# Kernel tuning notes

Hardware: AMD Instinct MI355X
Metric: run time of the kernel (lower is better)

The kernel has to match this reference:

```python
import jax, jax.numpy as jnp
import numpy as np

N_HEAD = 9
HEAD_DIM = 64
KV_PER_HEAD = 21  # 189 // 9
ROPE_BASE = 10000.0


def _rotate_half(x):
    # matches torch: x1 = first half (floor), x2 = rest; cat(-x2, x1)
    h = x.shape[-1] // 2
    return jnp.concatenate([-x[..., h:], x[..., :h]], axis=-1)


def _rope_cos_sin(T, dtype):
    inv_freq = 1.0 / (ROPE_BASE ** (jnp.arange(0, KV_PER_HEAD, 2, dtype=jnp.float32) / KV_PER_HEAD))  # [11]
    t = jnp.arange(T, dtype=jnp.float32)
    freqs = jnp.einsum('i,j->ij', t, inv_freq)          # [T, 11]
    emb = jnp.concatenate([freqs, freqs], axis=-1)      # [T, 22]
    cos = jnp.cos(emb)[:, :KV_PER_HEAD].astype(dtype)   # [T, 21]
    sin = jnp.sin(emb)[:, :KV_PER_HEAD].astype(dtype)
    return cos, sin


def setup_inputs() -> dict:
    key = jax.random.key(0)
    ks = jax.random.split(key, 5)
    B, T, C = 4, 2048, 576
    kv_dim = 189
    s = 0.02
    return {
        'x': jax.random.normal(ks[0], (B, T, C), dtype=jnp.float32),
        'Wq': jax.random.normal(ks[1], (C, C), dtype=jnp.float32) * s,
        'Wk': jax.random.normal(ks[2], (C, kv_dim), dtype=jnp.float32) * s,
        'Wv': jax.random.normal(ks[3], (C, kv_dim), dtype=jnp.float32) * s,
        'Wo': jax.random.normal(ks[4], (C, C), dtype=jnp.float32) * s,
    }


def reference(x, Wq, Wk, Wv, Wo):
    B, T, C = x.shape
    q = (x @ Wq).reshape(B, T, N_HEAD, HEAD_DIM).transpose(0, 2, 1, 3)      # [B,H,T,64]
    k = (x @ Wk).reshape(B, T, N_HEAD, KV_PER_HEAD).transpose(0, 2, 1, 3)   # [B,H,T,21]
    v = (x @ Wv).reshape(B, T, N_HEAD, KV_PER_HEAD).transpose(0, 2, 1, 3)   # [B,H,T,21]

    cos, sin = _rope_cos_sin(T, x.dtype)  # [T,21] each, broadcasts over B,H
    k_rot = k * cos + _rotate_half(k) * sin
    q_part = q[..., :KV_PER_HEAD]
    q_rot_part = q_part * cos + _rotate_half(q_part) * sin
    # q dims >= KV_PER_HEAD never touch nonzero K, so only the first 21 dims matter
    scale = 1.0 / np.sqrt(HEAD_DIM)
    scores = jnp.einsum('bhqd,bhkd->bhqk', q_rot_part, k_rot) * scale       # [B,H,T,T]
    causal = jnp.tril(jnp.ones((T, T), dtype=bool))
    scores = jnp.where(causal, scores, -1e9)
    attn = jax.nn.softmax(scores, axis=-1)
    y_small = jnp.einsum('bhqk,bhkd->bhqd', attn, v)                        # [B,H,T,21]
    # zero-pad up to head_dim (matches k_pad/v_pad construction)
    y = jnp.pad(y_small, ((0, 0), (0, 0), (0, 0), (0, HEAD_DIM - KV_PER_HEAD)))
    y = y.transpose(0, 2, 1, 3).reshape(B, T, C)
    return y @ Wo
```

## Files before the change

### kernel.cpp

```cpp
#include <hip/hip_runtime.h>
#include <hip/hip_bf16.h>

typedef unsigned short u16;
typedef unsigned int u32;
typedef __attribute__((ext_vector_type(8))) short bf16x8;
typedef __attribute__((ext_vector_type(4))) float f32x4;
typedef __attribute__((ext_vector_type(4))) int i32x4;

#define N_HEADS 9
#define T_SEQ 2048
#define BATCH 4
#define CDIM 576
#define ROWS (BATCH * T_SEQ)
#define NBH (BATCH * N_HEADS)
#define PART_SLOT ((size_t)NBH * T_SEQ * 32)

__device__ __forceinline__ u16 f2bf(float f) {
    u32 u = __float_as_uint(f);
    u32 r = u + 0x7FFFu + ((u >> 16) & 1u);
    return (u16)(r >> 16);
}
__device__ __forceinline__ float bf2f(u16 u) { return __uint_as_float(((u32)u) << 16); }
__device__ __forceinline__ u32 cvt_pk_bf16(float lo, float hi) {
    u32 r;
    asm("v_cvt_pk_bf16_f32 %0, %1, %2" : "=v"(r) : "v"(lo), "v"(hi));
    return r;
}
__device__ __forceinline__ float exp2_raw(float x) {
    float r;
    asm("v_exp_f32 %0, %1" : "=v"(r) : "v"(x));
    return r;
}

__global__ __launch_bounds__(256) void prep_wt(const float* __restrict__ Wq, const float* __restrict__ Wk,
                                               const float* __restrict__ Wv, const float* __restrict__ Wo,
                                               u16* __restrict__ WcT, u16* __restrict__ WoSubT,
                                               float* __restrict__ cosT, float* __restrict__ sinT) {
    int idx = blockIdx.x * 256 + threadIdx.x;
    if (idx < 576 * 576) {
        int n = idx / 576, k = idx - n * 576;
        float v;
        if (n < 189)      v = Wq[(size_t)k * 576 + (n / 21) * 64 + (n % 21)];
        else if (n < 378) v = Wk[(size_t)k * 189 + (n - 189)];
        else if (n < 567) v = Wv[(size_t)k * 189 + (n - 378)];
        else              v = 0.f;
        WcT[(size_t)n * 576 + k] = f2bf(v);
    }
    if (idx < 576 * 192) {
        int n = idx / 192, k = idx - n * 192;
        float v = 0.f;
        if (k < 189) v = Wo[(size_t)((k / 21) * 64 + (k % 21)) * 576 + n];
        WoSubT[(size_t)n * 192 + k] = f2bf(v);
    }
    if (idx < T_SEQ * 21) {
        int t = idx / 21, d = idx - t * 21;
        int i = (d < 11) ? d : d - 11;
        float e = (2.0f * (float)i) / 21.0f;
        float invf = exp2f(-e * 13.287712379549449f);
        float ang = (float)t * invf;
        cosT[idx] = cosf(ang);
        sinT[idx] = sinf(ang);
    }
}


template <int AF32, int OUTF32>
__global__ __launch_bounds__(256) void gemm_mfma(const void* __restrict__ Av, const u16* __restrict__ BT,
                                                 void* __restrict__ Cout, int K, int lda, int ldbt, int ldc) {
    __shared__ u16 As[128][32];
    __shared__ u16 Bs[64][32];
    const int tid = threadIdx.x;
    const int lane = tid & 63, w = tid >> 6;
    const int m0 = (blockIdx.x & 63) * 128, n0 = (blockIdx.x >> 6) * 64;
    const int k15 = lane & 15, g = lane >> 4;

    const int arow = tid >> 1;
    const int ac0 = (tid & 1) * 2;
    const int brow = tid >> 2, bc = tid & 3;

    f32x4 zero = {0.f, 0.f, 0.f, 0.f};
    f32x4 acc[2][4];
#pragma unroll
    for (int hf = 0; hf < 2; hf++)
#pragma unroll
        for (int n = 0; n < 4; n++) acc[hf][n] = zero;

    const float* Af = (const float*)Av;
    const u16*   Ab = (const u16*)Av;

    float4 af0, af1, af2, af3;
    i32x4 av0, av1;
    if (AF32) {
        const float* ap = &Af[(size_t)(m0 + arow) * lda + ac0 * 8];
        af0 = *(const float4*)&ap[0];
        af1 = *(const float4*)&ap[4];
        af2 = *(const float4*)&ap[8];
        af3 = *(const float4*)&ap[12];
    } else {
        av0 = *(const i32x4*)&Ab[(size_t)(m0 + arow) * lda + ac0 * 8];
        av1 = *(const i32x4*)&Ab[(size_t)(m0 + arow) * lda + (ac0 + 1) * 8];
    }
    i32x4 bv = *(const i32x4*)&BT[(size_t)(n0 + brow) * ldbt + bc * 8];

    for (int k0 = 0; k0 < K; k0 += 32) {
        __syncthreads();
        if (AF32) {
            i32x4 w0, w1;
            w0[0] = (int)cvt_pk_bf16(af0.x, af0.y); w0[1] = (int)cvt_pk_bf16(af0.z, af0.w);
            w0[2] = (int)cvt_pk_bf16(af1.x, af1.y); w0[3] = (int)cvt_pk_bf16(af1.z, af1.w);
            w1[0] = (int)cvt_pk_bf16(af2.x, af2.y); w1[1] = (int)cvt_pk_bf16(af2.z, af2.w);
            w1[2] = (int)cvt_pk_bf16(af3.x, af3.y); w1[3] = (int)cvt_pk_bf16(af3.z, af3.w);
            *(i32x4*)&As[arow][(ac0 ^ (arow & 3)) * 8] = w0;
            *(i32x4*)&As[arow][((ac0 + 1) ^ (arow & 3)) * 8] = w1;
        } else {
            *(i32x4*)&As[arow][(ac0 ^ (arow & 3)) * 8] = av0;
            *(i32x4*)&As[arow][((ac0 + 1) ^ (arow & 3)) * 8] = av1;
        }
        *(i32x4*)&Bs[brow][(bc ^ (brow & 3)) * 8] = bv;
        __syncthreads();
        int k1 = k0 + 32;
        if (k1 < K) {
            if (AF32) {
                const float* ap = &Af[(size_t)(m0 + arow) * lda + k1 + ac0 * 8];
                af0 = *(const float4*)&ap[0];
                af1 = *(const float4*)&ap[4];
                af2 = *(const float4*)&ap[8];
                af3 = *(const float4*)&ap[12];
            } else {
                av0 = *(const i32x4*)&Ab[(size_t)(m0 + arow) * lda + k1 + ac0 * 8];
                av1 = *(const i32x4*)&Ab[(size_t)(m0 + arow) * lda + k1 + (ac0 + 1) * 8];
            }
            bv = *(const i32x4*)&BT[(size_t)(n0 + brow) * ldbt + k1 + bc * 8];
        }
        const int ar0 = w * 32 + k15;
        bf16x8 a0 = *(const bf16x8*)&As[ar0][(g ^ (ar0 & 3)) * 8];
        bf16x8 a1 = *(const bf16x8*)&As[ar0 + 16][(g ^ (ar0 & 3)) * 8];
#pragma unroll
        for (int n = 0; n < 4; n++) {
            int br = n * 16 + k15;
            bf16x8 b = *(const bf16x8*)&Bs[br][(g ^ (br & 3)) * 8];
            acc[0][n] = __builtin_amdgcn_mfma_f32_16x16x32_bf16(a0, b, acc[0][n], 0, 0, 0);
            acc[1][n] = __builtin_amdgcn_mfma_f32_16x16x32_bf16(a1, b, acc[1][n], 0, 0, 0);
        }
    }
#pragma unroll
    for (int hf = 0; hf < 2; hf++)
#pragma unroll
        for (int n = 0; n < 4; n++)
#pragma unroll
            for (int i = 0; i < 4; i++) {
                int row = m0 + w * 32 + hf * 16 + g * 4 + i;
                int col = n0 + n * 16 + k15;
                float v = acc[hf][n][i];
                if (OUTF32) ((float*)Cout)[(size_t)row * ldc + col] = v;
                else        ((u16*)Cout)[(size_t)row * ldc + col] = f2bf(v);
            }
}


__global__ __launch_bounds__(256) void repack_qkv(const u16* __restrict__ qkv,
                                                  const float* __restrict__ cosT,
                                                  const float* __restrict__ sinT,
                                                  u16* __restrict__ Qp, u16* __restrict__ Kp,
                                                  u16* __restrict__ Vp) {
    __shared__ u16 Qs[64][40];
    __shared__ u16 Ksh[64][40];
    __shared__ u16 Vsh[64][40];
    const int tid = threadIdx.x;
    const int bh = blockIdx.y;
    const int b = bh / N_HEADS, h = bh - b * N_HEADS;
    const int t0 = blockIdx.x * 64;

    const int qa = (h * 21) & ~7,        qoff = h * 21 - qa;
    const int ka = (189 + h * 21) & ~7,  koff = 189 + h * 21 - ka;
    const int va = (378 + h * 21) & ~7,  voff = 378 + h * 21 - va;

#pragma unroll
    for (int it = 0; it < 3; ++it) {
        int idx = tid + it * 256;
        int row = idx / 12;
        int r12 = idx - row * 12;
        int stream = r12 >> 2, chunk = r12 & 3;
        int off = (stream == 0) ? qa : (stream == 1) ? ka : va;
        const u16* src = qkv + (size_t)(b * T_SEQ + t0 + row) * CDIM + off + chunk * 8;
        i32x4 v = *(const i32x4*)src;
        u16* dst = (stream == 0) ? &Qs[row][0] : (stream == 1) ? &Ksh[row][0] : &Vsh[row][0];
        *(i32x4*)&dst[chunk * 8] = v;
    }
    __syncthreads();

    const int r = tid >> 2, c = tid & 3;
    const int t = t0 + r;
    const float* cr = cosT + t * 21;
    const float* sr = sinT + t * 21;
    u32 wq[4] = {0, 0, 0, 0}, wk[4] = {0, 0, 0, 0};
    const float sc = 0.18033688011112042f;
#pragma unroll
    for (int j = 0; j < 8; j++) {
        int d = c * 8 + j;
        float vq = 0.f, vk = 0.f;
        if (d < 21) {
            int pd = (d < 11) ? d + 10 : d - 11;
            float cc = cr[d], ss = sr[d];
            float qv = bf2f(Qs[r][qoff + d]),  qp = bf2f(Qs[r][qoff + pd]);
            float kv = bf2f(Ksh[r][koff + d]), kp = bf2f(Ksh[r][koff + pd]);
            float rq = (d < 11) ? -qp : qp;
            float rk = (d < 11) ? -kp : kp;
            vq = (qv * cc + rq * ss) * sc;
            vk = kv * cc + rk * ss;
        }
        wq[j >> 1] |= (u32)f2bf(vq) << ((j & 1) * 16);
        wk[j >> 1] |= (u32)f2bf(vk) << ((j & 1) * 16);
    }
    size_t obase = ((size_t)bh * T_SEQ + t) * 32 + c * 8;
    i32x4 q4; q4[0] = (int)wq[0]; q4[1] = (int)wq[1]; q4[2] = (int)wq[2]; q4[3] = (int)wq[3];
    i32x4 k4; k4[0] = (int)wk[0]; k4[1] = (int)wk[1]; k4[2] = (int)wk[2]; k4[3] = (int)wk[3];
    *(i32x4*)&Qp[obase] = q4;
    *(i32x4*)&Kp[obase] = k4;

    const int dv = tid >> 3, tc = tid & 7;
    u32 wv[4];
#pragma unroll
    for (int j = 0; j < 4; j++) {
        u16 lo, hi;
        if (dv < 21)      { lo = Vsh[tc * 8 + j * 2][voff + dv]; hi = Vsh[tc * 8 + j * 2 + 1][voff + dv]; }
        else if (dv == 31){ lo = 0x3F80; hi = 0x3F80; }
        else              { lo = 0; hi = 0; }
        wv[j] = (u32)lo | ((u32)hi << 16);
    }
    i32x4 v4; v4[0] = (int)wv[0]; v4[1] = (int)wv[1]; v4[2] = (int)wv[2]; v4[3] = (int)wv[3];
    *(i32x4*)&Vp[((size_t)bh * 32 + dv) * T_SEQ + t0 + tc * 8] = v4;
}


__global__ __launch_bounds__(512) void attn_mfma(const u16* __restrict__ Qp,
                                                 const u16* __restrict__ Kp,
                                                 const u16* __restrict__ Vp,
                                                 u16* __restrict__ Ybuf,
                                                 u16* __restrict__ Part) {
    __shared__ u16 Ks[2][128][40];
    __shared__ u16 Vt[2][32][136];
    __shared__ u16 Pt[2][8][16][72];
    const int tid = threadIdx.x;
    const int lane = tid & 63, w = tid >> 6;
    const int bh = blockIdx.y;
    const int b = bh / N_HEADS, h = bh - b * N_HEADS;
    const int k15 = lane & 15, g = lane >> 4;

    int qt2 = 15, ci = blockIdx.x;
    for (int q = 15; q >= 0; --q) {
        int n = (q >> 2) + 1;
        if (ci < n) { qt2 = q; break; }
        ci -= n;
    }
    const int q0 = qt2 * 128;
    const int n128 = qt2 + 1;
    const int nc = (qt2 >> 2) + 1;
    const int u_begin = (ci * n128) / nc;
    const int u_end = ((ci + 1) * n128) / nc;

    const bool isK = (tid < 256);
    const int krow = (tid & 255) >> 2, kc = tid & 3;
    const int vrow = (tid & 255) >> 3, vc = tid & 7;
    const u16* Kg = Kp + (size_t)bh * 65536 + krow * 32 + kc * 8;
    const u16* Vg = Vp + (size_t)bh * 65536 + vrow * 2048 + vc * 8;

    bf16x8 qf = *(const bf16x8*)&Qp[(((size_t)bh << 11) + q0 + w * 16 + k15) * 32 + g * 8];

    f32x4 y0 = {0.f, 0.f, 0.f, 0.f}, y1 = {0.f, 0.f, 0.f, 0.f};
    const int qloc = (w & 3) * 16 + k15;
    const int kd = 2 * qt2 + (w >> 2);

    u32 koff = (u32)u_begin * 4096u;
    u32 voffu = (u32)u_begin * 128u;
    i32x4 r0, r1;
    if (isK) { r0 = *(const i32x4*)&Kg[koff];   r1 = *(const i32x4*)&Kg[koff + 2048]; }
    else     { r0 = *(const i32x4*)&Vg[voffu];  r1 = *(const i32x4*)&Vg[voffu + 64]; }
    if (isK) {
        *(i32x4*)&Ks[0][krow][kc * 8] = r0;
        *(i32x4*)&Ks[0][krow + 64][kc * 8] = r1;
    } else {
        *(i32x4*)&Vt[0][vrow][vc * 8] = r0;
        *(i32x4*)&Vt[0][vrow][vc * 8 + 64] = r1;
    }
    if (u_begin + 1 < u_end) {
        koff += 4096u; voffu += 128u;
        if (isK) { r0 = *(const i32x4*)&Kg[koff];   r1 = *(const i32x4*)&Kg[koff + 2048]; }
        else     { r0 = *(const i32x4*)&Vg[voffu];  r1 = *(const i32x4*)&Vg[voffu + 64]; }
    }

    int cur = 0;
    for (int u = u_begin; u < u_end; ++u) {
        __syncthreads();
        if (u + 1 < u_end) {
            if (isK) {
                *(i32x4*)&Ks[cur ^ 1][krow][kc * 8] = r0;
                *(i32x4*)&Ks[cur ^ 1][krow + 64][kc * 8] = r1;
            } else {
                *(i32x4*)&Vt[cur ^ 1][vrow][vc * 8] = r0;
                *(i32x4*)&Vt[cur ^ 1][vrow][vc * 8 + 64] = r1;
            }
            if (u + 2 < u_end) {
                koff += 4096u; voffu += 128u;
                if (isK) { r0 = *(const i32x4*)&Kg[koff];   r1 = *(const i32x4*)&Kg[koff + 2048]; }
                else     { r0 = *(const i32x4*)&Vg[voffu];  r1 = *(const i32x4*)&Vg[voffu + 64]; }
            }
        }

        const int kt0 = u * 2;
        const bool do0 = (kt0 <= kd);
        const bool do1 = (kt0 + 1 <= kd);

        if (do0) {
            f32x4 s0[4], s1[4];
            __builtin_amdgcn_s_setprio(1);
#pragma unroll
            for (int f = 0; f < 4; f++) {
                bf16x8 kf = *(const bf16x8*)&Ks[cur][f * 16 + k15][g * 8];
                f32x4 z = {0.f, 0.f, 0.f, 0.f};
                s0[f] = __builtin_amdgcn_mfma_f32_16x16x32_bf16(kf, qf, z, 0, 0, 0);
            }
            if (do1) {
#pragma unroll
                for (int f = 0; f < 4; f++) {
                    bf16x8 kf = *(const bf16x8*)&Ks[cur][64 + f * 16 + k15][g * 8];
                    f32x4 z = {0.f, 0.f, 0.f, 0.f};
                    s1[f] = __builtin_amdgcn_mfma_f32_16x16x32_bf16(kf, qf, z, 0, 0, 0);
                }
            }
            __builtin_amdgcn_s_setprio(0);

            if (kt0 == kd) {
#pragma unroll
                for (int f = 0; f < 4; f++)
#pragma unroll
                    for (int i = 0; i < 4; i++)
                        if (f * 16 + g * 4 + i > qloc) s0[f][i] = -16384.f;
            }
            if (do1 && kt0 + 1 == kd) {
#pragma unroll
                for (int f = 0; f < 4; f++)
#pragma unroll
                    for (int i = 0; i < 4; i++)
                        if (f * 16 + g * 4 + i > qloc) s1[f][i] = -16384.f;
            }

#pragma unroll
            for (int f = 0; f < 4; f++) {
                u32 lo = cvt_pk_bf16(exp2_raw(s0[f][0]), exp2_raw(s0[f][1]));
                u32 hi = cvt_pk_bf16(exp2_raw(s0[f][2]), exp2_raw(s0[f][3]));
                uint2 pk; pk.x = lo; pk.y = hi;
                *(uint2*)&Pt[0][w][k15][f * 16 + g * 4] = pk;
            }
            if (do1) {
#pragma unroll
                for (int f = 0; f < 4; f++) {
                    u32 lo = cvt_pk_bf16(exp2_raw(s1[f][0]), exp2_raw(s1[f][1]));
                    u32 hi = cvt_pk_bf16(exp2_raw(s1[f][2]), exp2_raw(s1[f][3]));
                    uint2 pk; pk.x = lo; pk.y = hi;
                    *(uint2*)&Pt[1][w][k15][f * 16 + g * 4] = pk;
                }
            }
            asm volatile("" ::: "memory");

            __builtin_amdgcn_s_setprio(1);
#pragma unroll
            for (int kh = 0; kh < 2; kh++) {
                bf16x8 pa = *(const bf16x8*)&Pt[0][w][k15][kh * 32 + g * 8];
                bf16x8 v0 = *(const bf16x8*)&Vt[cur][k15][kh * 32 + g * 8];
                bf16x8 v1 = *(const bf16x8*)&Vt[cur][16 + k15][kh * 32 + g * 8];
                y0 = __builtin_amdgcn_mfma_f32_16x16x32_bf16(pa, v0, y0, 0, 0, 0);
                y1 = __builtin_amdgcn_mfma_f32_16x16x32_bf16(pa, v1, y1, 0, 0, 0);
            }
            if (do1) {
#pragma unroll
                for (int kh = 0; kh < 2; kh++) {
                    bf16x8 pa = *(const bf16x8*)&Pt[1][w][k15][kh * 32 + g * 8];
                    bf16x8 v0 = *(const bf16x8*)&Vt[cur][k15][64 + kh * 32 + g * 8];
                    bf16x8 v1 = *(const bf16x8*)&Vt[cur][16 + k15][64 + kh * 32 + g * 8];
                    y0 = __builtin_amdgcn_mfma_f32_16x16x32_bf16(pa, v0, y0, 0, 0, 0);
                    y1 = __builtin_amdgcn_mfma_f32_16x16x32_bf16(pa, v1, y1, 0, 0, 0);
                }
            }
            __builtin_amdgcn_s_setprio(0);
            asm volatile("" ::: "memory");
        }
        cur ^= 1;
    }

    if (nc == 1) {
#pragma unroll
        for (int i = 0; i < 4; i++) {
            float li = __shfl(y1[i], (lane & 48) + 15);
            float inv = 1.0f / li;
            int rowY = b * T_SEQ + q0 + w * 16 + g * 4 + i;
            u16* yr = &Ybuf[(size_t)rowY * 192 + h * 21];
            yr[k15] = f2bf(y0[i] * inv);
            if (k15 < 5) yr[16 + k15] = f2bf(y1[i] * inv);
        }
    } else {
#pragma unroll
        for (int i = 0; i < 4; i++) {
            size_t pb = (size_t)ci * PART_SLOT +
                        (((size_t)bh << 11) + q0 + w * 16 + g * 4 + i) * 32;
            Part[pb + k15] = f2bf(y0[i]);
            Part[pb + 16 + k15] = f2bf(y1[i]);
        }
    }
}

__global__ __launch_bounds__(256) void attn_reduce(const u16* __restrict__ Part, u16* __restrict__ Ybuf) {
    int gid = blockIdx.x * 256 + threadIdx.x;
    int d = gid & 31;
    int rest = gid >> 5;
    int t = 512 + (rest % 1536);
    int bh = rest / 1536;
    int b = bh / N_HEADS, h = bh - b * N_HEADS;
    int nc = (t >> 9) + 1;
    size_t base = (((size_t)bh << 11) + t) * 32;
    float l = 0.f, v = 0.f;
    for (int ci = 0; ci < nc; ci++) {
        l += bf2f(Part[(size_t)ci * PART_SLOT + base + 31]);
        if (d < 21) v += bf2f(Part[(size_t)ci * PART_SLOT + base + d]);
    }
    if (d < 21) Ybuf[(size_t)(b * T_SEQ + t) * 192 + h * 21 + d] = f2bf(v / l);
}


extern "C" void kernel_launch(void* const* d_in, const int* in_sizes, int n_in,
                              void* d_out, int out_size, void* d_ws, size_t ws_size,
                              hipStream_t stream) {
    const float* x  = (const float*)d_in[0];
    const float* Wq = (const float*)d_in[1];
    const float* Wk = (const float*)d_in[2];
    const float* Wv = (const float*)d_in[3];
    const float* Wo = (const float*)d_in[4];
    float* out = (float*)d_out;

    char* p = (char*)d_ws;
    auto alloc = [&](size_t bytes) { char* r = p; p += (bytes + 255) & ~(size_t)255; return r; };
    u16*   QpKp   = (u16*)alloc((size_t)ROWS * CDIM * 2);
    u16*   qkv    = (u16*)alloc((size_t)ROWS * CDIM * 2);
    u16*   WcT    = (u16*)alloc((size_t)576 * 576 * 2);
    u16*   WoSubT = (u16*)alloc((size_t)576 * 192 * 2);
    float* cosT   = (float*)alloc((size_t)T_SEQ * 21 * 4);
    float* sinT   = (float*)alloc((size_t)T_SEQ * 21 * 4);
    u16*   Vp     = (u16*)alloc((size_t)NBH * 32 * T_SEQ * 2);
    u16*   Ybuf   = (u16*)alloc((size_t)ROWS * 192 * 2);
    u16*   Part   = (u16*)alloc((size_t)4 * PART_SLOT * 2);

    u16* Qp = QpKp;
    u16* Kp = QpKp + (size_t)NBH * T_SEQ * 32;

    prep_wt<<<dim3((576 * 576 + 255) / 256), dim3(256), 0, stream>>>(Wq, Wk, Wv, Wo, WcT, WoSubT, cosT, sinT);

    gemm_mfma<1, 0><<<dim3(64 * 9), dim3(256), 0, stream>>>((const void*)x, WcT, (void*)qkv, 576, 576, 576, 576);

    repack_qkv<<<dim3(T_SEQ / 64, NBH), dim3(256), 0, stream>>>(qkv, cosT, sinT, Qp, Kp, Vp);

    attn_mfma<<<dim3(40, NBH), dim3(512), 0, stream>>>(Qp, Kp, Vp, Ybuf, Part);
    attn_reduce<<<dim3(NBH * 1536 * 32 / 256), dim3(256), 0, stream>>>(Part, Ybuf);

    gemm_mfma<0, 1><<<dim3(64 * 9), dim3(256), 0, stream>>>((const void*)Ybuf, WoSubT, (void*)out, 192, 192, 192, 576);
}
```

Before: 77.88 us.

## Halve attention block to 4 waves, each handling two 16-row query fragments

The attention kernel now launches 256 threads instead of 512, and each wave processes 32 query rows as two 16-row fragments. Every K fragment loaded from shared memory and every V fragment is reused across both query fragments. Each thread now loads both K and V for the tile, where before threads were split between the two. This cuts LDS reads per MFMA and keeps more MFMAs in flight per wave, at the cost of more registers per thread and fewer waves per block available to hide latency.

Measured after the change: 79.58 us. 2.2% more time.

```diff
diff --git a/kernel.cpp b/kernel.cpp
--- a/kernel.cpp
+++ b/kernel.cpp
@@ -233,14 +233,14 @@
 }
 
 
-__global__ __launch_bounds__(512) void attn_mfma(const u16* __restrict__ Qp,
+__global__ __launch_bounds__(256) void attn_mfma(const u16* __restrict__ Qp,
                                                  const u16* __restrict__ Kp,
                                                  const u16* __restrict__ Vp,
                                                  u16* __restrict__ Ybuf,
                                                  u16* __restrict__ Part) {
     __shared__ u16 Ks[2][128][40];
     __shared__ u16 Vt[2][32][136];
-    __shared__ u16 Pt[2][8][16][72];
+    __shared__ u16 Pt[2][4][2][16][72];
     const int tid = threadIdx.x;
     const int lane = tid & 63, w = tid >> 6;
     const int bh = blockIdx.y;
@@ -259,152 +259,139 @@
     const int u_begin = (ci * n128) / nc;
     const int u_end = ((ci + 1) * n128) / nc;
 
-    const bool isK = (tid < 256);
-    const int krow = (tid & 255) >> 2, kc = tid & 3;
-    const int vrow = (tid & 255) >> 3, vc = tid & 7;
-    const u16* Kg = Kp + (size_t)bh * 65536 + krow * 32 + kc * 8;
+    const int krow = tid >> 1, kc = tid & 1;
+    const int vrow = tid >> 3, vc = tid & 7;
+    const u16* Kg = Kp + (size_t)bh * 65536 + krow * 32 + kc * 16;
     const u16* Vg = Vp + (size_t)bh * 65536 + vrow * 2048 + vc * 8;
 
-    bf16x8 qf = *(const bf16x8*)&Qp[(((size_t)bh << 11) + q0 + w * 16 + k15) * 32 + g * 8];
-
-    f32x4 y0 = {0.f, 0.f, 0.f, 0.f}, y1 = {0.f, 0.f, 0.f, 0.f};
-    const int qloc = (w & 3) * 16 + k15;
-    const int kd = 2 * qt2 + (w >> 2);
+    bf16x8 qfA = *(const bf16x8*)&Qp[(((size_t)bh << 11) + q0 + w * 32 + k15) * 32 + g * 8];
+    bf16x8 qfB = *(const bf16x8*)&Qp[(((size_t)bh << 11) + q0 + w * 32 + 16 + k15) * 32 + g * 8];
+
+    f32x4 y0A = {0.f, 0.f, 0.f, 0.f}, y1A = {0.f, 0.f, 0.f, 0.f};
+    f32x4 y0B = {0.f, 0.f, 0.f, 0.f}, y1B = {0.f, 0.f, 0.f, 0.f};
+    const int qlocA = ((2 * w) & 3) * 16 + k15;
+    const int qlocB = qlocA + 16;
+    const int kd = 2 * qt2 + (w >> 1);
 
     u32 koff = (u32)u_begin * 4096u;
     u32 voffu = (u32)u_begin * 128u;
-    i32x4 r0, r1;
-    if (isK) { r0 = *(const i32x4*)&Kg[koff];   r1 = *(const i32x4*)&Kg[koff + 2048]; }
-    else     { r0 = *(const i32x4*)&Vg[voffu];  r1 = *(const i32x4*)&Vg[voffu + 64]; }
-    if (isK) {
-        *(i32x4*)&Ks[0][krow][kc * 8] = r0;
-        *(i32x4*)&Ks[0][krow + 64][kc * 8] = r1;
-    } else {
-        *(i32x4*)&Vt[0][vrow][vc * 8] = r0;
-        *(i32x4*)&Vt[0][vrow][vc * 8 + 64] = r1;
-    }
+    i32x4 kr0 = *(const i32x4*)&Kg[koff];
+    i32x4 kr1 = *(const i32x4*)&Kg[koff + 8];
+    i32x4 vr0 = *(const i32x4*)&Vg[voffu];
+    i32x4 vr1 = *(const i32x4*)&Vg[voffu + 64];
+    *(i32x4*)&Ks[0][krow][kc * 16] = kr0;
+    *(i32x4*)&Ks[0][krow][kc * 16 + 8] = kr1;
+    *(i32x4*)&Vt[0][vrow][vc * 8] = vr0;
+    *(i32x4*)&Vt[0][vrow][vc * 8 + 64] = vr1;
     if (u_begin + 1 < u_end) {
         koff += 4096u; voffu += 128u;
-        if (isK) { r0 = *(const i32x4*)&Kg[koff];   r1 = *(const i32x4*)&Kg[koff + 2048]; }
-        else     { r0 = *(const i32x4*)&Vg[voffu];  r1 = *(const i32x4*)&Vg[voffu + 64]; }
+        kr0 = *(const i32x4*)&Kg[koff];
+        kr1 = *(const i32x4*)&Kg[koff + 8];
+        vr0 = *(const i32x4*)&Vg[voffu];
+        vr1 = *(const i32x4*)&Vg[voffu + 64];
     }
 
     int cur = 0;
     for (int u = u_begin; u < u_end; ++u) {
         __syncthreads();
         if (u + 1 < u_end) {
-            if (isK) {
-                *(i32x4*)&Ks[cur ^ 1][krow][kc * 8] = r0;
-                *(i32x4*)&Ks[cur ^ 1][krow + 64][kc * 8] = r1;
-            } else {
-                *(i32x4*)&Vt[cur ^ 1][vrow][vc * 8] = r0;
-                *(i32x4*)&Vt[cur ^ 1][vrow][vc * 8 + 64] = r1;
-            }
+            *(i32x4*)&Ks[cur ^ 1][krow][kc * 16] = kr0;
+            *(i32x4*)&Ks[cur ^ 1][krow][kc * 16 + 8] = kr1;
+            *(i32x4*)&Vt[cur ^ 1][vrow][vc * 8] = vr0;
+            *(i32x4*)&Vt[cur ^ 1][vrow][vc * 8 + 64] = vr1;
             if (u + 2 < u_end) {
                 koff += 4096u; voffu += 128u;
-                if (isK) { r0 = *(const i32x4*)&Kg[koff];   r1 = *(const i32x4*)&Kg[koff + 2048]; }
-                else     { r0 = *(const i32x4*)&Vg[voffu];  r1 = *(const i32x4*)&Vg[voffu + 64]; }
-            }
-        }
-
-        const int kt0 = u * 2;
-        const bool do0 = (kt0 <= kd);
-        const bool do1 = (kt0 + 1 <= kd);
-
-        if (do0) {
-            f32x4 s0[4], s1[4];
-            __builtin_amdgcn_s_setprio(1);
-#pragma unroll
-            for (int f = 0; f < 4; f++) {
-                bf16x8 kf = *(const bf16x8*)&Ks[cur][f * 16 + k15][g * 8];
-                f32x4 z = {0.f, 0.f, 0.f, 0.f};
-                s0[f] = __builtin_amdgcn_mfma_f32_16x16x32_bf16(kf, qf, z, 0, 0, 0);
-            }
-            if (do1) {
+                kr0 = *(const i32x4*)&Kg[koff];
+                kr1 = *(const i32x4*)&Kg[koff + 8];
+                vr0 = *(const i32x4*)&Vg[voffu];
+                vr1 = *(const i32x4*)&Vg[voffu + 64];
+            }
+        }
+
+#pragma unroll
+        for (int sub = 0; sub < 2; ++sub) {
+            const int kt = u * 2 + sub;
+            if (kt <= kd) {
+                f32x4 sA[4], sB[4];
+                __builtin_amdgcn_s_setprio(1);
 #pragma unroll
                 for (int f = 0; f < 4; f++) {
-                    bf16x8 kf = *(const bf16x8*)&Ks[cur][64 + f * 16 + k15][g * 8];
+                    bf16x8 kf = *(const bf16x8*)&Ks[cur][sub * 64 + f * 16 + k15][g * 8];
                     f32x4 z = {0.f, 0.f, 0.f, 0.f};
-                    s1[f] = __builtin_amdgcn_mfma_f32_16x16x32_bf16(kf, qf, z, 0, 0, 0);
+                    sA[f] = __builtin_amdgcn_mfma_f32_16x16x32_bf16(kf, qfA, z, 0, 0, 0);
+                    sB[f] = __builtin_amdgcn_mfma_f32_16x16x32_bf16(kf, qfB, z, 0, 0, 0);
                 }
-            }
-            __builtin_amdgcn_s_setprio(0);
-
-            if (kt0 == kd) {
-#pragma unroll
-                for (int f = 0; f < 4; f++)
-#pragma unroll
-                    for (int i = 0; i < 4; i++)
-                        if (f * 16 + g * 4 + i > qloc) s0[f][i] = -16384.f;
-            }
-            if (do1 && kt0 + 1 == kd) {
-#pragma unroll
-                for (int f = 0; f < 4; f++)
-#pragma unroll
-                    for (int i = 0; i < 4; i++)
-                        if (f * 16 + g * 4 + i > qloc) s1[f][i] = -16384.f;
-            }
-
-#pragma unroll
-            for (int f = 0; f < 4; f++) {
-                u32 lo = cvt_pk_bf16(exp2_raw(s0[f][0]), exp2_raw(s0[f][1]));
-                u32 hi = cvt_pk_bf16(exp2_raw(s0[f][2]), exp2_raw(s0[f][3]));
-                uint2 pk; pk.x = lo; pk.y = hi;
-                *(uint2*)&Pt[0][w][k15][f * 16 + g * 4] = pk;
-            }
-            if (do1) {
+                __builtin_amdgcn_s_setprio(0);
+
+                if (kt == kd) {
+#pragma unroll
+                    for (int f = 0; f < 4; f++)
+#pragma unroll
+                        for (int i = 0; i < 4; i++) {
+                            if (f * 16 + g * 4 + i > qlocA) sA[f][i] = -16384.f;
+                            if (f * 16 + g * 4 + i > qlocB) sB[f][i] = -16384.f;
+                        }
+                }
+
 #pragma unroll
                 for (int f = 0; f < 4; f++) {
-                    u32 lo = cvt_pk_bf16(exp2_raw(s1[f][0]), exp2_raw(s1[f][1]));
-                    u32 hi = cvt_pk_bf16(exp2_raw(s1[f][2]), exp2_raw(s1[f][3]));
-                    uint2 pk; pk.x = lo; pk.y = hi;
-                    *(uint2*)&Pt[1][w][k15][f * 16 + g * 4] = pk;
+                    u32 loA = cvt_pk_bf16(exp2_raw(sA[f][0]), exp2_raw(sA[f][1]));
+                    u32 hiA = cvt_pk_bf16(exp2_raw(sA[f][2]), exp2_raw(sA[f][3]));
+                    uint2 pkA; pkA.x = loA; pkA.y = hiA;
+                    *(uint2*)&Pt[sub][w][0][k15][f * 16 + g * 4] = pkA;
+                    u32 loB = cvt_pk_bf16(exp2_raw(sB[f][0]), exp2_raw(sB[f][1]));
+                    u32 hiB = cvt_pk_bf16(exp2_raw(sB[f][2]), exp2_raw(sB[f][3]));
+                    uint2 pkB; pkB.x = loB; pkB.y = hiB;
+                    *(uint2*)&Pt[sub][w][1][k15][f * 16 + g * 4] = pkB;
                 }
-            }
-            asm volatile("" ::: "memory");
-
-            __builtin_amdgcn_s_setprio(1);
-#pragma unroll
-            for (int kh = 0; kh < 2; kh++) {
-                bf16x8 pa = *(const bf16x8*)&Pt[0][w][k15][kh * 32 + g * 8];
-                bf16x8 v0 = *(const bf16x8*)&Vt[cur][k15][kh * 32 + g * 8];
-                bf16x8 v1 = *(const bf16x8*)&Vt[cur][16 + k15][kh * 32 + g * 8];
-                y0 = __builtin_amdgcn_mfma_f32_16x16x32_bf16(pa, v0, y0, 0, 0, 0);
-                y1 = __builtin_amdgcn_mfma_f32_16x16x32_bf16(pa, v1, y1, 0, 0, 0);
-            }
-            if (do1) {
+                asm volatile("" ::: "memory");
+
+                __builtin_amdgcn_s_setprio(1);
 #pragma unroll
                 for (int kh = 0; kh < 2; kh++) {
-                    bf16x8 pa = *(const bf16x8*)&Pt[1][w][k15][kh * 32 + g * 8];
-                    bf16x8 v0 = *(const bf16x8*)&Vt[cur][k15][64 + kh * 32 + g * 8];
-                    bf16x8 v1 = *(const bf16x8*)&Vt[cur][16 + k15][64 + kh * 32 + g * 8];
-                    y0 = __builtin_amdgcn_mfma_f32_16x16x32_bf16(pa, v0, y0, 0, 0, 0);
-                    y1 = __builtin_amdgcn_mfma_f32_16x16x32_bf16(pa, v1, y1, 0, 0, 0);
+                    bf16x8 paA = *(const bf16x8*)&Pt[sub][w][0][k15][kh * 32 + g * 8];
+                    bf16x8 paB = *(const bf16x8*)&Pt[sub][w][1][k15][kh * 32 + g * 8];
+                    bf16x8 v0 = *(const bf16x8*)&Vt[cur][k15][sub * 64 + kh * 32 + g * 8];
+                    bf16x8 v1 = *(const bf16x8*)&Vt[cur][16 + k15][sub * 64 + kh * 32 + g * 8];
+                    y0A = __builtin_amdgcn_mfma_f32_16x16x32_bf16(paA, v0, y0A, 0, 0, 0);
+                    y1A = __builtin_amdgcn_mfma_f32_16x16x32_bf16(paA, v1, y1A, 0, 0, 0);
+                    y0B = __builtin_amdgcn_mfma_f32_16x16x32_bf16(paB, v0, y0B, 0, 0, 0);
+                    y1B = __builtin_amdgcn_mfma_f32_16x16x32_bf16(paB, v1, y1B, 0, 0, 0);
                 }
-            }
-            __builtin_amdgcn_s_setprio(0);
-            asm volatile("" ::: "memory");
+                __builtin_amdgcn_s_setprio(0);
+                asm volatile("" ::: "memory");
+            }
         }
         cur ^= 1;
     }
 
     if (nc == 1) {
 #pragma unroll
-        for (int i = 0; i < 4; i++) {
-            float li = __shfl(y1[i], (lane & 48) + 15);
-            float inv = 1.0f / li;
-            int rowY = b * T_SEQ + q0 + w * 16 + g * 4 + i;
-            u16* yr = &Ybuf[(size_t)rowY * 192 + h * 21];
-            yr[k15] = f2bf(y0[i] * inv);
-            if (k15 < 5) yr[16 + k15] = f2bf(y1[i] * inv);
+        for (int fr = 0; fr < 2; fr++) {
+            f32x4 yy0 = fr ? y0B : y0A;
+            f32x4 yy1 = fr ? y1B : y1A;
+#pragma unroll
+            for (int i = 0; i < 4; i++) {
+                float li = __shfl(yy1[i], (lane & 48) + 15);
+                float inv = 1.0f / li;
+                int rowY = b * T_SEQ + q0 + w * 32 + fr * 16 + g * 4 + i;
+                u16* yr = &Ybuf[(size_t)rowY * 192 + h * 21];
+                yr[k15] = f2bf(yy0[i] * inv);
+                if (k15 < 5) yr[16 + k15] = f2bf(yy1[i] * inv);
+            }
         }
     } else {
 #pragma unroll
-        for (int i = 0; i < 4; i++) {
-            size_t pb = (size_t)ci * PART_SLOT +
-                        (((size_t)bh << 11) + q0 + w * 16 + g * 4 + i) * 32;
-            Part[pb + k15] = f2bf(y0[i]);
-            Part[pb + 16 + k15] = f2bf(y1[i]);
+        for (int fr = 0; fr < 2; fr++) {
+            f32x4 yy0 = fr ? y0B : y0A;
+            f32x4 yy1 = fr ? y1B : y1A;
+#pragma unroll
+            for (int i = 0; i < 4; i++) {
+                size_t pb = (size_t)ci * PART_SLOT +
+                            (((size_t)bh << 11) + q0 + w * 32 + fr * 16 + g * 4 + i) * 32;
+                Part[pb + k15] = f2bf(yy0[i]);
+                Part[pb + 16 + k15] = f2bf(yy1[i]);
+            }
         }
     }
 }
@@ -458,7 +445,7 @@
 
     repack_qkv<<<dim3(T_SEQ / 64, NBH), dim3(256), 0, stream>>>(qkv, cosT, sinT, Qp, Kp, Vp);
 
-    attn_mfma<<<dim3(40, NBH), dim3(512), 0, stream>>>(Qp, Kp, Vp, Ybuf, Part);
+    attn_mfma<<<dim3(40, NBH), dim3(256), 0, stream>>>(Qp, Kp, Vp, Ybuf, Part);
     attn_reduce<<<dim3(NBH * 1536 * 32 / 256), dim3(256), 0, stream>>>(Part, Ybuf);
 
     gemm_mfma<0, 1><<<dim3(64 * 9), dim3(256), 0, stream>>>((const void*)Ybuf, WoSubT, (void*)out, 192, 192, 192, 576);
```
